# Kernel optimization log

Hardware: AMD Instinct MI355X
Metric: run time of the kernel (lower is better)

The kernel has to match this reference:

```python
import jax, jax.numpy as jnp
import numpy as np

N = 4096
F_OUT = 512
R = 474
IN_RELS = 500
N_EDGES = 131072
NEG_INF = -9e15


def setup_inputs() -> dict:
    key = jax.random.key(0)
    ks = jax.random.split(key, 8)
    inp = jax.random.normal(ks[0], (N, F_OUT), dtype=jnp.float32)
    rel = jax.random.normal(ks[1], (R, IN_RELS), dtype=jnp.float32)
    w_rel = jax.random.normal(ks[2], (IN_RELS,), dtype=jnp.float32) * (1.0 / np.sqrt(IN_RELS))
    bias = jnp.zeros((F_OUT,), dtype=jnp.float32)
    edge_src = jax.random.randint(ks[3], (N_EDGES,), 0, N, dtype=jnp.int64)
    edge_dst = jax.random.randint(ks[4], (N_EDGES,), 0, N, dtype=jnp.int64)
    rel_edge_id = jnp.arange(N_EDGES, dtype=jnp.int64)  # one relation entry per edge
    rel_idx = jax.random.randint(ks[5], (N_EDGES,), 0, R, dtype=jnp.int64)
    # adj is the additive softmax mask: 0 where an edge (or self-loop) exists, -9e15 elsewhere
    adj = jnp.full((N, N), NEG_INF, dtype=jnp.float32)
    adj = adj.at[edge_src, edge_dst].set(0.0).at[edge_dst, edge_src].set(0.0)
    adj = adj.at[jnp.arange(N), jnp.arange(N)].set(0.0)
    return {"input": inp, "rel": rel, "adj": adj, "w_rel": w_rel, "bias": bias,
            "edge_src": edge_src, "edge_dst": edge_dst,
            "rel_edge_id": rel_edge_id, "rel_idx": rel_idx}


def reference(input, rel, adj, w_rel, bias, edge_src, edge_dst, rel_edge_id, rel_idx):
    # Conv1d(in_rels, 1, k=1, bias=False) over transposed rel == linear score per relation type
    seq_fts_rel = rel @ w_rel                      # [R]
    # per-edge max over that edge's relation-type scores (replaces the python loop)
    edge_vals = jax.ops.segment_max(seq_fts_rel[rel_idx], rel_edge_id,
                                    num_segments=edge_src.shape[0])  # [E]
    n = adj.shape[0]
    logits = jnp.zeros((n, n), dtype=adj.dtype)
    logits = logits.at[edge_src, edge_dst].set(edge_vals).at[edge_dst, edge_src].set(edge_vals)
    coefs = jax.nn.softmax(jax.nn.relu(logits) + adj, axis=1)  # dropout is identity at eval
    ret = coefs @ input + bias                     # [N, F_OUT]
    return jax.nn.elu(ret)                         # concat=True branch
```

## Files before the change

### kernel.cpp

```cpp
#include <hip/hip_runtime.h>
#include <hip/hip_bf16.h>

typedef float f32x4 __attribute__((ext_vector_type(4)));

__device__ __forceinline__ float bflo(unsigned p) { return __uint_as_float(p << 16); }
__device__ __forceinline__ float bfhi(unsigned p) { return __uint_as_float(p & 0xFFFF0000u); }

__device__ __forceinline__ unsigned pack2(float a, float b) {
    unsigned ua = __float_as_uint(a); ua += 0x7FFFu + ((ua >> 16) & 1u);
    unsigned ub = __float_as_uint(b); ub += 0x7FFFu + ((ub >> 16) & 1u);
    return ((ua >> 16) & 0xFFFFu) | (ub & 0xFFFF0000u);
}

__device__ __forceinline__ int geti(const int* __restrict__ a, int e, int f) {
    return f ? a[2 * e] : a[e];
}

__device__ __forceinline__ void probe(const int* __restrict__ a7, const int* __restrict__ a8,
                                      int& f, const int*& ridx) {
    int arange7;
    if (a7[1] == 1 && a7[2] == 2)                                  { f = 0; arange7 = 1; }
    else if (a7[1] == 0 && a7[2] == 1 && a7[3] == 0 && a7[4] == 2) { f = 1; arange7 = 1; }
    else { arange7 = 0; f = (a8[1] == 1 && a8[2] == 2) ? 0 : 1; }
    ridx = arange7 ? a8 : a7;
}

__global__ __launch_bounds__(256) void k_pre(const float* __restrict__ rel,
                                             const float* __restrict__ wr,
                                             const float* __restrict__ inp,
                                             float* __restrict__ seq,
                                             unsigned* __restrict__ cnt,
                                             uint2* __restrict__ inpb,
                                             int R, int inr, int n, int nF) {
    __shared__ float part[256];
    int b = blockIdx.x, t = threadIdx.x;
    int nz = (n + 255) / 256;
    if (b < R) {
        float s = 0.f;
        for (int c = t; c < inr; c += 256) s += rel[(size_t)b * inr + c] * wr[c];
        part[t] = s;
        __syncthreads();
        for (int d = 128; d; d >>= 1) {
            if (t < d) part[t] += part[t + d];
            __syncthreads();
        }
        if (t == 0) seq[b] = part[0];
    } else if (b < R + nz) {
        int i = (b - R) * 256 + t;
        if (i < n) cnt[i] = 0u;
    } else {
        int gid = (b - R - nz) * 256 + t;
        if (gid < nF / 4) {
            f32x4 v = ((const f32x4*)inp)[gid];
            inpb[gid] = make_uint2(pack2(v.x, v.y), pack2(v.z, v.w));
        }
    }
}

__global__ __launch_bounds__(256) void k_fill(const int* __restrict__ src, const int* __restrict__ dst,
                                              const int* __restrict__ a7, const int* __restrict__ a8,
                                              unsigned* __restrict__ cnt, unsigned* __restrict__ ent,
                                              int ne, int stride) {
    int e = blockIdx.x * 256 + threadIdx.x;
    if (e >= ne) return;
    int f; const int* ridx; probe(a7, a8, f, ridx);
    int a = geti(src, e, f), b = geti(dst, e, f);
    unsigned p = atomicAdd(&cnt[a], 1u);
    if (p < (unsigned)stride)
        __builtin_nontemporal_store(((unsigned)(e + 1) << 12) | (unsigned)b,
                                    &ent[(size_t)a * stride + p]);
    unsigned q = atomicAdd(&cnt[b], 1u);
    if (q < (unsigned)stride)
        __builtin_nontemporal_store(((unsigned)(ne + e + 1) << 12) | (unsigned)a,
                                    &ent[(size_t)b * stride + q]);
}

__global__ __launch_bounds__(256) void k_dedup(const unsigned* __restrict__ cnt,
                                               const unsigned* __restrict__ ent,
                                               const float* __restrict__ seq,
                                               const int* __restrict__ a7, const int* __restrict__ a8,
                                               uint2* __restrict__ ccw, unsigned* __restrict__ cm,
                                               int n, int ne, int stride) {
    __shared__ unsigned best[4096];
    __shared__ unsigned sp[256];
    __shared__ int      ncol[258];
    __shared__ float    nw[258];
    __shared__ unsigned cntn;
    int row = blockIdx.x, tid = threadIdx.x;

    int f; const int* ridx; probe(a7, a8, f, ridx);

    for (int i = tid; i < n; i += 256) best[i] = 0u;
    if (tid == 0) cntn = 0u;
    __syncthreads();

    int deg = (int)cnt[row];
    if (deg > stride) deg = stride;
    if (deg > 256)    deg = 256;
    const unsigned* erow = ent + (size_t)row * stride;
    if (tid < deg) sp[tid] = erow[tid];
    __syncthreads();

    if (tid < deg) atomicMax(&best[sp[tid] & 0xFFFu], sp[tid]);
    __syncthreads();

    if (tid < deg) {
        unsigned pk = sp[tid];
        unsigned col = pk & 0xFFFu;
        if (best[col] == pk) {
            unsigned key = pk >> 12;
            int e = (key > (unsigned)ne) ? (int)(key - (unsigned)ne - 1u) : (int)(key - 1u);
            float v = seq[geti(ridx, e, f)];
            unsigned s = atomicAdd(&cntn, 1u);
            ncol[s] = (int)col;
            nw[s] = expf(fmaxf(v, 0.f));
        }
    }
    if (tid == 0 && best[row] == 0u) {
        unsigned s = atomicAdd(&cntn, 1u);
        ncol[s] = row;
        nw[s] = 1.0f;
    }
    __syncthreads();

    int m = (int)cntn;
    if (m > 256) m = 256;
    float den = 0.f;
    for (int s = 0; s < m; ++s) den += nw[s];
    float inv = 1.0f / den;
    if (tid < m) ccw[(size_t)row * stride + tid] = make_uint2((unsigned)ncol[tid],
                                                              __float_as_uint(nw[tid] * inv));
    if (tid == 0) cm[row] = (unsigned)m;
}

__global__ __launch_bounds__(256) void k_main(const uint2* __restrict__ ccw,
                                              const unsigned* __restrict__ cm,
                                              const uint4* __restrict__ inpb,
                                              const float* __restrict__ bias,
                                              float* __restrict__ out,
                                              int F, int stride) {
    __shared__ uint2 sl[4][258];
    int wid = threadIdx.x >> 6, lane = threadIdx.x & 63;
    int row = (blockIdx.x << 2) + wid;

    int m = (int)cm[row];
    if (m > 256) m = 256;
    for (int t = lane; t < m; t += 64) sl[wid][t] = ccw[(size_t)row * stride + t];
    __syncthreads();

    int nq = F >> 3;
    const uint2* L = sl[wid];
    f32x4 acA = {0.f, 0.f, 0.f, 0.f}, acB = acA;
    int s = 0;
    for (; s + 3 < m; s += 4) {
        uint2 e0 = L[s], e1 = L[s + 1], e2 = L[s + 2], e3 = L[s + 3];
        uint4 q0 = inpb[(size_t)e0.x * nq + lane];
        uint4 q1 = inpb[(size_t)e1.x * nq + lane];
        uint4 q2 = inpb[(size_t)e2.x * nq + lane];
        uint4 q3 = inpb[(size_t)e3.x * nq + lane];
        float w0 = __uint_as_float(e0.y), w1 = __uint_as_float(e1.y);
        float w2 = __uint_as_float(e2.y), w3 = __uint_as_float(e3.y);
        acA.x += w0 * bflo(q0.x); acA.y += w0 * bfhi(q0.x); acA.z += w0 * bflo(q0.y); acA.w += w0 * bfhi(q0.y);
        acB.x += w0 * bflo(q0.z); acB.y += w0 * bfhi(q0.z); acB.z += w0 * bflo(q0.w); acB.w += w0 * bfhi(q0.w);
        acA.x += w1 * bflo(q1.x); acA.y += w1 * bfhi(q1.x); acA.z += w1 * bflo(q1.y); acA.w += w1 * bfhi(q1.y);
        acB.x += w1 * bflo(q1.z); acB.y += w1 * bfhi(q1.z); acB.z += w1 * bflo(q1.w); acB.w += w1 * bfhi(q1.w);
        acA.x += w2 * bflo(q2.x); acA.y += w2 * bfhi(q2.x); acA.z += w2 * bflo(q2.y); acA.w += w2 * bfhi(q2.y);
        acB.x += w2 * bflo(q2.z); acB.y += w2 * bfhi(q2.z); acB.z += w2 * bflo(q2.w); acB.w += w2 * bfhi(q2.w);
        acA.x += w3 * bflo(q3.x); acA.y += w3 * bfhi(q3.x); acA.z += w3 * bflo(q3.y); acA.w += w3 * bfhi(q3.y);
        acB.x += w3 * bflo(q3.z); acB.y += w3 * bfhi(q3.z); acB.z += w3 * bflo(q3.w); acB.w += w3 * bfhi(q3.w);
    }
    for (; s < m; ++s) {
        uint2 e0 = L[s];
        uint4 q0 = inpb[(size_t)e0.x * nq + lane];
        float w0 = __uint_as_float(e0.y);
        acA.x += w0 * bflo(q0.x); acA.y += w0 * bfhi(q0.x); acA.z += w0 * bflo(q0.y); acA.w += w0 * bfhi(q0.y);
        acB.x += w0 * bflo(q0.z); acB.y += w0 * bfhi(q0.z); acB.z += w0 * bflo(q0.w); acB.w += w0 * bfhi(q0.w);
    }
    const f32x4* b4 = (const f32x4*)bias;
    f32x4 r0 = acA + b4[2 * lane];
    f32x4 r1 = acB + b4[2 * lane + 1];
    r0.x = (r0.x > 0.f) ? r0.x : expm1f(r0.x);
    r0.y = (r0.y > 0.f) ? r0.y : expm1f(r0.y);
    r0.z = (r0.z > 0.f) ? r0.z : expm1f(r0.z);
    r0.w = (r0.w > 0.f) ? r0.w : expm1f(r0.w);
    r1.x = (r1.x > 0.f) ? r1.x : expm1f(r1.x);
    r1.y = (r1.y > 0.f) ? r1.y : expm1f(r1.y);
    r1.z = (r1.z > 0.f) ? r1.z : expm1f(r1.z);
    r1.w = (r1.w > 0.f) ? r1.w : expm1f(r1.w);
    f32x4* orow = (f32x4*)out + (size_t)row * (F >> 2);
    __builtin_nontemporal_store(r0, &orow[2 * lane]);
    __builtin_nontemporal_store(r1, &orow[2 * lane + 1]);
}

extern "C" void kernel_launch(void* const* d_in, const int* in_sizes, int n_in,
                              void* d_out, int out_size, void* d_ws, size_t ws_size,
                              hipStream_t stream) {
    const float* inp  = (const float*)d_in[0];
    const float* rel  = (const float*)d_in[1];
    const float* wrel = (const float*)d_in[3];
    const float* bias = (const float*)d_in[4];
    const int* esrc = (const int*)d_in[5];
    const int* edst = (const int*)d_in[6];
    const int* a7   = (const int*)d_in[7];
    const int* a8   = (const int*)d_in[8];

    const int F   = in_sizes[4];
    const int n   = in_sizes[0] / F;
    const int inr = in_sizes[3];
    const int R   = in_sizes[1] / inr;
    const int ne  = in_sizes[5];
    const int nF  = n * F;

    char* w = (char*)d_ws;
    size_t o = 0;
    float*    seq  = (float*)(w + o);    o += ((size_t)R * 4 + 255) & ~255ull;
    unsigned* cnt  = (unsigned*)(w + o); o += ((size_t)n * 4 + 255) & ~255ull;
    unsigned* cm   = (unsigned*)(w + o); o += ((size_t)n * 4 + 255) & ~255ull;
    uint2*    inpb = (uint2*)(w + o);    o += (size_t)nF * 2;
    size_t avail = (ws_size > o) ? (ws_size - o) / ((size_t)n * 12) : 0;
    int stride = (avail >= 256) ? 256 : (avail >= 192) ? 192 : (avail >= 128) ? 128 : 96;
    unsigned* ent = (unsigned*)(w + o); o += (size_t)n * stride * 4;
    uint2*    ccw = (uint2*)(w + o);

    int nz = (n + 255) / 256;
    int nconv = (nF / 4 + 255) / 256;
    hipLaunchKernelGGL(k_pre,   dim3(R + nz + nconv),   dim3(256), 0, stream,
                       rel, wrel, inp, seq, cnt, inpb, R, inr, n, nF);
    hipLaunchKernelGGL(k_fill,  dim3((ne + 255) / 256), dim3(256), 0, stream,
                       esrc, edst, a7, a8, cnt, ent, ne, stride);
    hipLaunchKernelGGL(k_dedup, dim3(n),                dim3(256), 0, stream,
                       cnt, ent, seq, a7, a8, ccw, cm, n, ne, stride);
    hipLaunchKernelGGL(k_main,  dim3(n / 4),            dim3(256), 0, stream,
                       ccw, cm, (const uint4*)inpb, bias, (float*)d_out, F, stride);
}
```

Measured before the change: 65.86 us.

## Fuse dedup into aggregation kernel with per-wave O(deg^2) duplicate check

Merges the per-row dedup kernel and the gather/aggregate kernel into one launch. Each wave handles one row and finds duplicate columns with a pairwise scan over the row's entries in shared memory, replacing the 4096-entry shared best array. Normalization by the softmax denominator moves to the final accumulator scale. The bf16 conversion of the input moves from k_pre into the fill kernel, and the intermediate ccw/cm buffers are removed. The trade is one less launch and less global traffic against quadratic per-row compare work and longer serial loops within each wave.

```diff
diff --git a/kernel.cpp b/kernel.cpp
--- a/kernel.cpp
+++ b/kernel.cpp
@@ -27,14 +27,11 @@
 
 __global__ __launch_bounds__(256) void k_pre(const float* __restrict__ rel,
                                              const float* __restrict__ wr,
-                                             const float* __restrict__ inp,
                                              float* __restrict__ seq,
                                              unsigned* __restrict__ cnt,
-                                             uint2* __restrict__ inpb,
-                                             int R, int inr, int n, int nF) {
+                                             int R, int inr, int n) {
     __shared__ float part[256];
     int b = blockIdx.x, t = threadIdx.x;
-    int nz = (n + 255) / 256;
     if (b < R) {
         float s = 0.f;
         for (int c = t; c < inr; c += 256) s += rel[(size_t)b * inr + c] * wr[c];
@@ -45,11 +42,34 @@
             __syncthreads();
         }
         if (t == 0) seq[b] = part[0];
-    } else if (b < R + nz) {
+    } else {
         int i = (b - R) * 256 + t;
         if (i < n) cnt[i] = 0u;
+    }
+}
+
+__global__ __launch_bounds__(256) void k_fill(const int* __restrict__ src, const int* __restrict__ dst,
+                                              const int* __restrict__ a7, const int* __restrict__ a8,
+                                              const float* __restrict__ inp,
+                                              unsigned* __restrict__ cnt, unsigned* __restrict__ ent,
+                                              uint2* __restrict__ inpb,
+                                              int ne, int stride, int gedge, int nF) {
+    int b = blockIdx.x, t = threadIdx.x;
+    if (b < gedge) {
+        int e = b * 256 + t;
+        if (e >= ne) return;
+        int f; const int* ridx; probe(a7, a8, f, ridx);
+        int a = geti(src, e, f), d = geti(dst, e, f);
+        unsigned p = atomicAdd(&cnt[a], 1u);
+        if (p < (unsigned)stride)
+            __builtin_nontemporal_store(((unsigned)(e + 1) << 12) | (unsigned)d,
+                                        &ent[(size_t)a * stride + p]);
+        unsigned q = atomicAdd(&cnt[d], 1u);
+        if (q < (unsigned)stride)
+            __builtin_nontemporal_store(((unsigned)(ne + e + 1) << 12) | (unsigned)a,
+                                        &ent[(size_t)d * stride + q]);
     } else {
-        int gid = (b - R - nz) * 256 + t;
+        int gid = (b - gedge) * 256 + t;
         if (gid < nF / 4) {
             f32x4 v = ((const f32x4*)inp)[gid];
             inpb[gid] = make_uint2(pack2(v.x, v.y), pack2(v.z, v.w));
@@ -57,99 +77,65 @@
     }
 }
 
-__global__ __launch_bounds__(256) void k_fill(const int* __restrict__ src, const int* __restrict__ dst,
-                                              const int* __restrict__ a7, const int* __restrict__ a8,
-                                              unsigned* __restrict__ cnt, unsigned* __restrict__ ent,
-                                              int ne, int stride) {
-    int e = blockIdx.x * 256 + threadIdx.x;
-    if (e >= ne) return;
-    int f; const int* ridx; probe(a7, a8, f, ridx);
-    int a = geti(src, e, f), b = geti(dst, e, f);
-    unsigned p = atomicAdd(&cnt[a], 1u);
-    if (p < (unsigned)stride)
-        __builtin_nontemporal_store(((unsigned)(e + 1) << 12) | (unsigned)b,
-                                    &ent[(size_t)a * stride + p]);
-    unsigned q = atomicAdd(&cnt[b], 1u);
-    if (q < (unsigned)stride)
-        __builtin_nontemporal_store(((unsigned)(ne + e + 1) << 12) | (unsigned)a,
-                                    &ent[(size_t)b * stride + q]);
-}
-
-__global__ __launch_bounds__(256) void k_dedup(const unsigned* __restrict__ cnt,
+__global__ __launch_bounds__(256) void k_fused(const unsigned* __restrict__ cnt,
                                                const unsigned* __restrict__ ent,
                                                const float* __restrict__ seq,
                                                const int* __restrict__ a7, const int* __restrict__ a8,
-                                               uint2* __restrict__ ccw, unsigned* __restrict__ cm,
-                                               int n, int ne, int stride) {
-    __shared__ unsigned best[4096];
-    __shared__ unsigned sp[256];
-    __shared__ int      ncol[258];
-    __shared__ float    nw[258];
-    __shared__ unsigned cntn;
-    int row = blockIdx.x, tid = threadIdx.x;
+                                               const uint4* __restrict__ inpb,
+                                               const float* __restrict__ bias,
+                                               float* __restrict__ out,
+                                               int n, int F, int ne, int stride) {
+    __shared__ unsigned sp[4][256];
+    __shared__ uint2    lst[4][260];
+    __shared__ unsigned cntn[4];
+    __shared__ int      diag[4];
+    int wid = threadIdx.x >> 6, lane = threadIdx.x & 63;
+    int row = (blockIdx.x << 2) + wid;
 
     int f; const int* ridx; probe(a7, a8, f, ridx);
 
-    for (int i = tid; i < n; i += 256) best[i] = 0u;
-    if (tid == 0) cntn = 0u;
+    if (lane == 0) { cntn[wid] = 0u; diag[wid] = 0; }
     __syncthreads();
 
     int deg = (int)cnt[row];
     if (deg > stride) deg = stride;
     if (deg > 256)    deg = 256;
     const unsigned* erow = ent + (size_t)row * stride;
-    if (tid < deg) sp[tid] = erow[tid];
-    __syncthreads();
-
-    if (tid < deg) atomicMax(&best[sp[tid] & 0xFFFu], sp[tid]);
-    __syncthreads();
-
-    if (tid < deg) {
-        unsigned pk = sp[tid];
+    for (int t = lane; t < deg; t += 64) sp[wid][t] = erow[t];
+    __syncthreads();
+
+    for (int t = lane; t < deg; t += 64) {
+        unsigned pk = sp[wid][t];
         unsigned col = pk & 0xFFFu;
-        if (best[col] == pk) {
+        if (col == (unsigned)row) diag[wid] = 1;
+        bool win = true;
+        for (int j = 0; j < deg; ++j) {
+            unsigned pj = sp[wid][j];
+            if (((pj ^ pk) & 0xFFFu) == 0u && pj > pk) { win = false; break; }
+        }
+        if (win) {
             unsigned key = pk >> 12;
             int e = (key > (unsigned)ne) ? (int)(key - (unsigned)ne - 1u) : (int)(key - 1u);
             float v = seq[geti(ridx, e, f)];
-            unsigned s = atomicAdd(&cntn, 1u);
-            ncol[s] = (int)col;
-            nw[s] = expf(fmaxf(v, 0.f));
-        }
-    }
-    if (tid == 0 && best[row] == 0u) {
-        unsigned s = atomicAdd(&cntn, 1u);
-        ncol[s] = row;
-        nw[s] = 1.0f;
-    }
-    __syncthreads();
-
-    int m = (int)cntn;
-    if (m > 256) m = 256;
+            unsigned s = atomicAdd(&cntn[wid], 1u);
+            lst[wid][s] = make_uint2(col, __float_as_uint(expf(fmaxf(v, 0.f))));
+        }
+    }
+    __syncthreads();
+    if (lane == 0 && !diag[wid]) {
+        unsigned s = atomicAdd(&cntn[wid], 1u);
+        lst[wid][s] = make_uint2((unsigned)row, __float_as_uint(1.0f));
+    }
+    __syncthreads();
+
+    int m = (int)cntn[wid];
+    if (m > 260) m = 260;
     float den = 0.f;
-    for (int s = 0; s < m; ++s) den += nw[s];
+    for (int s = 0; s < m; ++s) den += __uint_as_float(lst[wid][s].y);
     float inv = 1.0f / den;
-    if (tid < m) ccw[(size_t)row * stride + tid] = make_uint2((unsigned)ncol[tid],
-                                                              __float_as_uint(nw[tid] * inv));
-    if (tid == 0) cm[row] = (unsigned)m;
-}
-
-__global__ __launch_bounds__(256) void k_main(const uint2* __restrict__ ccw,
-                                              const unsigned* __restrict__ cm,
-                                              const uint4* __restrict__ inpb,
-                                              const float* __restrict__ bias,
-                                              float* __restrict__ out,
-                                              int F, int stride) {
-    __shared__ uint2 sl[4][258];
-    int wid = threadIdx.x >> 6, lane = threadIdx.x & 63;
-    int row = (blockIdx.x << 2) + wid;
-
-    int m = (int)cm[row];
-    if (m > 256) m = 256;
-    for (int t = lane; t < m; t += 64) sl[wid][t] = ccw[(size_t)row * stride + t];
-    __syncthreads();
 
     int nq = F >> 3;
-    const uint2* L = sl[wid];
+    const uint2* L = lst[wid];
     f32x4 acA = {0.f, 0.f, 0.f, 0.f}, acB = acA;
     int s = 0;
     for (; s + 3 < m; s += 4) {
@@ -177,8 +163,8 @@
         acB.x += w0 * bflo(q0.z); acB.y += w0 * bfhi(q0.z); acB.z += w0 * bflo(q0.w); acB.w += w0 * bfhi(q0.w);
     }
     const f32x4* b4 = (const f32x4*)bias;
-    f32x4 r0 = acA + b4[2 * lane];
-    f32x4 r1 = acB + b4[2 * lane + 1];
+    f32x4 r0 = acA * inv + b4[2 * lane];
+    f32x4 r1 = acB * inv + b4[2 * lane + 1];
     r0.x = (r0.x > 0.f) ? r0.x : expm1f(r0.x);
     r0.y = (r0.y > 0.f) ? r0.y : expm1f(r0.y);
     r0.z = (r0.z > 0.f) ? r0.z : expm1f(r0.z);
@@ -215,21 +201,18 @@
     size_t o = 0;
     float*    seq  = (float*)(w + o);    o += ((size_t)R * 4 + 255) & ~255ull;
     unsigned* cnt  = (unsigned*)(w + o); o += ((size_t)n * 4 + 255) & ~255ull;
-    unsigned* cm   = (unsigned*)(w + o); o += ((size_t)n * 4 + 255) & ~255ull;
     uint2*    inpb = (uint2*)(w + o);    o += (size_t)nF * 2;
-    size_t avail = (ws_size > o) ? (ws_size - o) / ((size_t)n * 12) : 0;
+    size_t avail = (ws_size > o) ? (ws_size - o) / ((size_t)n * 4) : 0;
     int stride = (avail >= 256) ? 256 : (avail >= 192) ? 192 : (avail >= 128) ? 128 : 96;
-    unsigned* ent = (unsigned*)(w + o); o += (size_t)n * stride * 4;
-    uint2*    ccw = (uint2*)(w + o);
+    unsigned* ent = (unsigned*)(w + o);
 
     int nz = (n + 255) / 256;
+    int gedge = (ne + 255) / 256;
     int nconv = (nF / 4 + 255) / 256;
-    hipLaunchKernelGGL(k_pre,   dim3(R + nz + nconv),   dim3(256), 0, stream,
-                       rel, wrel, inp, seq, cnt, inpb, R, inr, n, nF);
-    hipLaunchKernelGGL(k_fill,  dim3((ne + 255) / 256), dim3(256), 0, stream,
-                       esrc, edst, a7, a8, cnt, ent, ne, stride);
-    hipLaunchKernelGGL(k_dedup, dim3(n),                dim3(256), 0, stream,
-                       cnt, ent, seq, a7, a8, ccw, cm, n, ne, stride);
-    hipLaunchKernelGGL(k_main,  dim3(n / 4),            dim3(256), 0, stream,
-                       ccw, cm, (const uint4*)inpb, bias, (float*)d_out, F, stride);
-}
+    hipLaunchKernelGGL(k_pre,   dim3(R + nz),          dim3(256), 0, stream,
+                       rel, wrel, seq, cnt, R, inr, n);
+    hipLaunchKernelGGL(k_fill,  dim3(gedge + nconv),   dim3(256), 0, stream,
+                       esrc, edst, a7, a8, inp, cnt, ent, (uint2*)inpb, ne, stride, gedge, nF);
+    hipLaunchKernelGGL(k_fused, dim3(n / 4),           dim3(256), 0, stream,
+                       cnt, ent, seq, a7, a8, (const uint4*)inpb, bias, (float*)d_out, n, F, ne, stride);
+}
```

Result: slower. 70.87 us (+7.6%).

## Fuse dedup and aggregation kernels, split neighbor sum across four waves

Applied to the files above, without the earlier changes.

Merges the per-row dedup/softmax-weight kernel with the gather-aggregate kernel, so the compacted neighbor list stays in shared memory and is never written to or reread from global memory. Each 256-thread block now handles one row, with its four waves taking interleaved neighbors and combining partial sums through shared memory before normalization, bias and ELU. This removes a kernel launch and the ccw/cm round trip, but each row now pays an extra reduction barrier and only one wave does the final store.

```diff
diff --git a/kernel.cpp b/kernel.cpp
--- a/kernel.cpp
+++ b/kernel.cpp
@@ -75,17 +75,18 @@
                                     &ent[(size_t)b * stride + q]);
 }
 
-__global__ __launch_bounds__(256) void k_dedup(const unsigned* __restrict__ cnt,
-                                               const unsigned* __restrict__ ent,
-                                               const float* __restrict__ seq,
-                                               const int* __restrict__ a7, const int* __restrict__ a8,
-                                               uint2* __restrict__ ccw, unsigned* __restrict__ cm,
-                                               int n, int ne, int stride) {
+__global__ __launch_bounds__(256) void k_dm(const unsigned* __restrict__ cnt,
+                                            const unsigned* __restrict__ ent,
+                                            const float* __restrict__ seq,
+                                            const int* __restrict__ a7, const int* __restrict__ a8,
+                                            const uint4* __restrict__ inpb,
+                                            const float* __restrict__ bias,
+                                            float* __restrict__ out,
+                                            int n, int F, int ne, int stride) {
     __shared__ unsigned best[4096];
-    __shared__ unsigned sp[256];
-    __shared__ int      ncol[258];
-    __shared__ float    nw[258];
+    __shared__ uint2    lst[260];
     __shared__ unsigned cntn;
+    __shared__ f32x4    red[3][64][2];
     int row = blockIdx.x, tid = threadIdx.x;
 
     int f; const int* ridx; probe(a7, a8, f, ridx);
@@ -97,63 +98,39 @@
     int deg = (int)cnt[row];
     if (deg > stride) deg = stride;
     if (deg > 256)    deg = 256;
-    const unsigned* erow = ent + (size_t)row * stride;
-    if (tid < deg) sp[tid] = erow[tid];
-    __syncthreads();
-
-    if (tid < deg) atomicMax(&best[sp[tid] & 0xFFFu], sp[tid]);
-    __syncthreads();
-
+    unsigned pk = 0u;
     if (tid < deg) {
-        unsigned pk = sp[tid];
-        unsigned col = pk & 0xFFFu;
-        if (best[col] == pk) {
-            unsigned key = pk >> 12;
-            int e = (key > (unsigned)ne) ? (int)(key - (unsigned)ne - 1u) : (int)(key - 1u);
-            float v = seq[geti(ridx, e, f)];
-            unsigned s = atomicAdd(&cntn, 1u);
-            ncol[s] = (int)col;
-            nw[s] = expf(fmaxf(v, 0.f));
-        }
-    }
+        pk = ent[(size_t)row * stride + tid];
+        atomicMax(&best[pk & 0xFFFu], pk);
+    }
+    __syncthreads();
+
+    if (tid < deg && best[pk & 0xFFFu] == pk) {
+        unsigned key = pk >> 12;
+        int e = (key > (unsigned)ne) ? (int)(key - (unsigned)ne - 1u) : (int)(key - 1u);
+        float v = seq[geti(ridx, e, f)];
+        unsigned s = atomicAdd(&cntn, 1u);
+        lst[s] = make_uint2(pk & 0xFFFu, __float_as_uint(expf(fmaxf(v, 0.f))));
+    }
+    __syncthreads();
     if (tid == 0 && best[row] == 0u) {
         unsigned s = atomicAdd(&cntn, 1u);
-        ncol[s] = row;
-        nw[s] = 1.0f;
+        lst[s] = make_uint2((unsigned)row, __float_as_uint(1.0f));
     }
     __syncthreads();
 
     int m = (int)cntn;
-    if (m > 256) m = 256;
+    if (m > 260) m = 260;
     float den = 0.f;
-    for (int s = 0; s < m; ++s) den += nw[s];
+    for (int s = 0; s < m; ++s) den += __uint_as_float(lst[s].y);
     float inv = 1.0f / den;
-    if (tid < m) ccw[(size_t)row * stride + tid] = make_uint2((unsigned)ncol[tid],
-                                                              __float_as_uint(nw[tid] * inv));
-    if (tid == 0) cm[row] = (unsigned)m;
-}
-
-__global__ __launch_bounds__(256) void k_main(const uint2* __restrict__ ccw,
-                                              const unsigned* __restrict__ cm,
-                                              const uint4* __restrict__ inpb,
-                                              const float* __restrict__ bias,
-                                              float* __restrict__ out,
-                                              int F, int stride) {
-    __shared__ uint2 sl[4][258];
-    int wid = threadIdx.x >> 6, lane = threadIdx.x & 63;
-    int row = (blockIdx.x << 2) + wid;
-
-    int m = (int)cm[row];
-    if (m > 256) m = 256;
-    for (int t = lane; t < m; t += 64) sl[wid][t] = ccw[(size_t)row * stride + t];
-    __syncthreads();
-
+
+    int wid = tid >> 6, lane = tid & 63;
     int nq = F >> 3;
-    const uint2* L = sl[wid];
     f32x4 acA = {0.f, 0.f, 0.f, 0.f}, acB = acA;
-    int s = 0;
-    for (; s + 3 < m; s += 4) {
-        uint2 e0 = L[s], e1 = L[s + 1], e2 = L[s + 2], e3 = L[s + 3];
+    int s = wid;
+    for (; s + 12 < m; s += 16) {
+        uint2 e0 = lst[s], e1 = lst[s + 4], e2 = lst[s + 8], e3 = lst[s + 12];
         uint4 q0 = inpb[(size_t)e0.x * nq + lane];
         uint4 q1 = inpb[(size_t)e1.x * nq + lane];
         uint4 q2 = inpb[(size_t)e2.x * nq + lane];
@@ -169,27 +146,36 @@
         acA.x += w3 * bflo(q3.x); acA.y += w3 * bfhi(q3.x); acA.z += w3 * bflo(q3.y); acA.w += w3 * bfhi(q3.y);
         acB.x += w3 * bflo(q3.z); acB.y += w3 * bfhi(q3.z); acB.z += w3 * bflo(q3.w); acB.w += w3 * bfhi(q3.w);
     }
-    for (; s < m; ++s) {
-        uint2 e0 = L[s];
+    for (; s < m; s += 4) {
+        uint2 e0 = lst[s];
         uint4 q0 = inpb[(size_t)e0.x * nq + lane];
         float w0 = __uint_as_float(e0.y);
         acA.x += w0 * bflo(q0.x); acA.y += w0 * bfhi(q0.x); acA.z += w0 * bflo(q0.y); acA.w += w0 * bfhi(q0.y);
         acB.x += w0 * bflo(q0.z); acB.y += w0 * bfhi(q0.z); acB.z += w0 * bflo(q0.w); acB.w += w0 * bfhi(q0.w);
     }
-    const f32x4* b4 = (const f32x4*)bias;
-    f32x4 r0 = acA + b4[2 * lane];
-    f32x4 r1 = acB + b4[2 * lane + 1];
-    r0.x = (r0.x > 0.f) ? r0.x : expm1f(r0.x);
-    r0.y = (r0.y > 0.f) ? r0.y : expm1f(r0.y);
-    r0.z = (r0.z > 0.f) ? r0.z : expm1f(r0.z);
-    r0.w = (r0.w > 0.f) ? r0.w : expm1f(r0.w);
-    r1.x = (r1.x > 0.f) ? r1.x : expm1f(r1.x);
-    r1.y = (r1.y > 0.f) ? r1.y : expm1f(r1.y);
-    r1.z = (r1.z > 0.f) ? r1.z : expm1f(r1.z);
-    r1.w = (r1.w > 0.f) ? r1.w : expm1f(r1.w);
-    f32x4* orow = (f32x4*)out + (size_t)row * (F >> 2);
-    __builtin_nontemporal_store(r0, &orow[2 * lane]);
-    __builtin_nontemporal_store(r1, &orow[2 * lane + 1]);
+    if (wid > 0) {
+        red[wid - 1][lane][0] = acA;
+        red[wid - 1][lane][1] = acB;
+    }
+    __syncthreads();
+    if (wid == 0) {
+        f32x4 sA = acA + red[0][lane][0] + red[1][lane][0] + red[2][lane][0];
+        f32x4 sB = acB + red[0][lane][1] + red[1][lane][1] + red[2][lane][1];
+        const f32x4* b4 = (const f32x4*)bias;
+        f32x4 r0 = sA * inv + b4[2 * lane];
+        f32x4 r1 = sB * inv + b4[2 * lane + 1];
+        r0.x = (r0.x > 0.f) ? r0.x : expm1f(r0.x);
+        r0.y = (r0.y > 0.f) ? r0.y : expm1f(r0.y);
+        r0.z = (r0.z > 0.f) ? r0.z : expm1f(r0.z);
+        r0.w = (r0.w > 0.f) ? r0.w : expm1f(r0.w);
+        r1.x = (r1.x > 0.f) ? r1.x : expm1f(r1.x);
+        r1.y = (r1.y > 0.f) ? r1.y : expm1f(r1.y);
+        r1.z = (r1.z > 0.f) ? r1.z : expm1f(r1.z);
+        r1.w = (r1.w > 0.f) ? r1.w : expm1f(r1.w);
+        f32x4* orow = (f32x4*)out + (size_t)row * (F >> 2);
+        __builtin_nontemporal_store(r0, &orow[2 * lane]);
+        __builtin_nontemporal_store(r1, &orow[2 * lane + 1]);
+    }
 }
 
 extern "C" void kernel_launch(void* const* d_in, const int* in_sizes, int n_in,
@@ -215,21 +201,17 @@
     size_t o = 0;
     float*    seq  = (float*)(w + o);    o += ((size_t)R * 4 + 255) & ~255ull;
     unsigned* cnt  = (unsigned*)(w + o); o += ((size_t)n * 4 + 255) & ~255ull;
-    unsigned* cm   = (unsigned*)(w + o); o += ((size_t)n * 4 + 255) & ~255ull;
     uint2*    inpb = (uint2*)(w + o);    o += (size_t)nF * 2;
-    size_t avail = (ws_size > o) ? (ws_size - o) / ((size_t)n * 12) : 0;
+    size_t avail = (ws_size > o) ? (ws_size - o) / ((size_t)n * 4) : 0;
     int stride = (avail >= 256) ? 256 : (avail >= 192) ? 192 : (avail >= 128) ? 128 : 96;
-    unsigned* ent = (unsigned*)(w + o); o += (size_t)n * stride * 4;
-    uint2*    ccw = (uint2*)(w + o);
+    unsigned* ent = (unsigned*)(w + o);
 
     int nz = (n + 255) / 256;
     int nconv = (nF / 4 + 255) / 256;
-    hipLaunchKernelGGL(k_pre,   dim3(R + nz + nconv),   dim3(256), 0, stream,
+    hipLaunchKernelGGL(k_pre,  dim3(R + nz + nconv),   dim3(256), 0, stream,
                        rel, wrel, inp, seq, cnt, inpb, R, inr, n, nF);
-    hipLaunchKernelGGL(k_fill,  dim3((ne + 255) / 256), dim3(256), 0, stream,
+    hipLaunchKernelGGL(k_fill, dim3((ne + 255) / 256), dim3(256), 0, stream,
                        esrc, edst, a7, a8, cnt, ent, ne, stride);
-    hipLaunchKernelGGL(k_dedup, dim3(n),                dim3(256), 0, stream,
-                       cnt, ent, seq, a7, a8, ccw, cm, n, ne, stride);
-    hipLaunchKernelGGL(k_main,  dim3(n / 4),            dim3(256), 0, stream,
-                       ccw, cm, (const uint4*)inpb, bias, (float*)d_out, F, stride);
-}
+    hipLaunchKernelGGL(k_dm,   dim3(n),                dim3(256), 0, stream,
+                       cnt, ent, seq, a7, a8, (const uint4*)inpb, bias, (float*)d_out, n, F, ne, stride);
+}
```

After: 63.61 us. 3.4% less time.
